# Performance work log

Measured on AMD Instinct MI355X. Metric: run time of the kernel, lower is better.

## Reference

```python
import jax, jax.numpy as jnp
import numpy as np
from jax.scipy.linalg import expm

DIM = 64
TIMESTEPS = 1000
BATCH = 1024


def setup_inputs() -> dict:
    key = jax.random.key(0)
    k1, k2 = jax.random.split(key)
    inputs = jax.random.normal(k1, (BATCH, TIMESTEPS, DIM), dtype=jnp.float32)
    # Kernel: skew-symmetric (oscillatory) + small decay so expm(kernel*t) stays
    # bounded for t up to TIMESTEPS-1 (a random dense kernel would overflow).
    a = jax.random.normal(k2, (DIM, DIM), dtype=jnp.float32)
    kernel = 0.01 * (a - a.T) - 0.002 * jnp.eye(DIM, dtype=jnp.float32)
    return {"inputs": inputs, "kernel": kernel}


def reference(inputs, kernel):
    # matrix_exponentials[t] = expm(kernel * t), t = 0..T-1  -> [T, dim, dim]
    ts = jnp.arange(TIMESTEPS, dtype=kernel.dtype)
    mexp = jax.vmap(expm)(kernel[None, :, :] * ts[:, None, None])
    # trajs = einsum('tij,bj->bti'): propagate initial state inputs[:, 0, :]
    x0 = inputs[:, 0, :]  # [B, dim]
    return jnp.einsum('tij,bj->bti', mexp, x0)  # [B, T, dim]
```

## Files before the change

### kernel.cpp

```cpp
#include <hip/hip_runtime.h>

#define NMAT 1000
#define SA_PAD 68
#define LDM 72

typedef short short8 __attribute__((ext_vector_type(8)));
typedef float floatx4 __attribute__((ext_vector_type(4)));
typedef unsigned short ushortx4 __attribute__((ext_vector_type(4)));

__device__ __forceinline__ unsigned short f2bf(float f) {
    unsigned int u = __float_as_uint(f);
    u += 0x7fffu + ((u >> 16) & 1u);
    return (unsigned short)(u >> 16);
}

__device__ __forceinline__ void mm_core(const float* __restrict__ sA,
                                        const float* __restrict__ sB,
                                        int r0, int c0, float acc[4][4])
{
#pragma unroll
    for (int k = 0; k < 64; k += 4) {
        float4 b0 = *(const float4*)&sB[(k + 0) * SA_PAD + c0];
        float4 b1 = *(const float4*)&sB[(k + 1) * SA_PAD + c0];
        float4 b2 = *(const float4*)&sB[(k + 2) * SA_PAD + c0];
        float4 b3 = *(const float4*)&sB[(k + 3) * SA_PAD + c0];
#pragma unroll
        for (int u = 0; u < 4; ++u) {
            float4 a = *(const float4*)&sA[(r0 + u) * SA_PAD + k];
            acc[u][0] += a.x * b0.x + a.y * b1.x + a.z * b2.x + a.w * b3.x;
            acc[u][1] += a.x * b0.y + a.y * b1.y + a.z * b2.y + a.w * b3.y;
            acc[u][2] += a.x * b0.z + a.y * b1.z + a.z * b2.z + a.w * b3.z;
            acc[u][3] += a.x * b0.w + a.y * b1.w + a.z * b2.w + a.w * b3.w;
        }
    }
}

__device__ __forceinline__ void stageLDS(float* __restrict__ s, const float* __restrict__ g, int tid)
{
#pragma unroll
    for (int q = 0; q < 4; ++q) {
        int i4 = tid + 256 * q;
        int r = i4 >> 4, c4 = (i4 & 15) * 4;
        *(float4*)&s[r * SA_PAD + c4] = *(const float4*)&g[i4 * 4];
    }
}

__global__ __launch_bounds__(256) void k_build(const float* __restrict__ K,
                                               float* __restrict__ ws)
{
    __shared__ __align__(16) float smem[6 * 64 * SA_PAD];
    float* tab = ws;
    const int tid = threadIdx.x;

#pragma unroll
    for (int q = 0; q < 4; ++q) {
        int i4 = tid + 256 * q;
        int r = i4 >> 4, c4 = (i4 & 15) * 4;
        *(float4*)&smem[r * SA_PAD + c4] = *(const float4*)&K[i4 * 4];
        float4 id = {0.f, 0.f, 0.f, 0.f};
        if (r >= c4 && r < c4 + 4) ((float*)&id)[r - c4] = 1.f;
        *(float4*)&tab[r * 64 + c4] = id;
    }

    const float c1_ = 1.f, c2_ = 0.5f, c3_ = 1.f / 6.f, c4_ = 1.f / 24.f, c5_ = 1.f / 120.f,
                c6_ = 1.f / 720.f, c7_ = 1.f / 5040.f, c8_ = 1.f / 40320.f, c9_ = 1.f / 362880.f,
                c10_ = 1.f / 3628800.f, c11_ = 1.f / 39916800.f, c12_ = 1.f / 479001600.f;

    const signed char SD[14]  = {1, 2, 3, 5, 4, 5, 0, 1, 2, 3, 4, 5, 0, 1};
    const signed char SAi[14] = {0, 1, 1, 4, 5, 4, 5, 0, 1, 2, 3, 4, 5, 0};
    const signed char SBi[14] = {0, 0, 1, 3, 3, 4, 5, 0, 1, 2, 3, 4, 5, 0};
    const signed char SE[14]  = {-1, -1, -1, 0, 1, -1, -1, -1, -1, -1, -1, -1, -1, -1};
    const short       STt[14] = {-1, -1, -1, -1, 1, 2, 4, 8, 16, 32, 64, 128, 256, 512};

    const int r0 = (tid >> 4) * 4, c0 = (tid & 15) * 4;

#pragma unroll 1
    for (int st = 0; st < 14; ++st) {
        if (st == 3) {
            __syncthreads();
#pragma unroll
            for (int s = 0; s < 16; ++s) {
                int idx = tid + 256 * s;
                int r = idx >> 6, c = idx & 63;
                smem[4 * (64 * SA_PAD) + r * SA_PAD + c] =
                      c12_ * smem[3 * (64 * SA_PAD) + r * SA_PAD + c] + (r == c ? c8_ : 0.f)
                    + c9_  * smem[0 * (64 * SA_PAD) + r * SA_PAD + c]
                    + c10_ * smem[1 * (64 * SA_PAD) + r * SA_PAD + c]
                    + c11_ * smem[2 * (64 * SA_PAD) + r * SA_PAD + c];
            }
        }
        __syncthreads();
        const float* A = smem + (int)SAi[st] * (64 * SA_PAD);
        const float* B = smem + (int)SBi[st] * (64 * SA_PAD);
        float acc[4][4] = {};
        mm_core(A, B, r0, c0, acc);

        float cI = 0.f, cK = 0.f, cT2 = 0.f, cT3 = 0.f;
        const int epi = SE[st];
        if (epi == 0) { cI = c4_; cK = c5_; cT2 = c6_; cT3 = c7_; }
        if (epi == 1) { cI = 1.f; cK = c1_; cT2 = c2_; cT3 = c3_; }

        float* D = smem + (int)SD[st] * (64 * SA_PAD);
        float* tp = (STt[st] >= 0) ? (tab + (size_t)STt[st] * 4096) : nullptr;
#pragma unroll
        for (int u = 0; u < 4; ++u) {
            int r = r0 + u;
            float o[4];
#pragma unroll
            for (int v = 0; v < 4; ++v) {
                int c = c0 + v;
                float val = acc[u][v];
                if (epi >= 0) {
                    val += (r == c ? cI : 0.f)
                         + cK  * smem[0 * (64 * SA_PAD) + r * SA_PAD + c]
                         + cT2 * smem[1 * (64 * SA_PAD) + r * SA_PAD + c]
                         + cT3 * smem[2 * (64 * SA_PAD) + r * SA_PAD + c];
                }
                o[v] = val;
            }
            float4 vv = {o[0], o[1], o[2], o[3]};
            *(float4*)&D[r * SA_PAD + c0] = vv;
            if (tp) *(float4*)&tp[r * 64 + c0] = vv;
        }
    }
}

__global__ __launch_bounds__(256) void k_pows(float* __restrict__ ws)
{
    __shared__ __align__(16) float s0[64 * SA_PAD], s1[64 * SA_PAD], s2[64 * SA_PAD];
    const int t = blockIdx.x;
    if (__popc(t) < 2) return;
    float* tab = ws;
    const int tid = threadIdx.x;
    const int r0 = (tid >> 4) * 4, c0 = (tid & 15) * 4;

    float* P = s0;
    float* Bs = s1;
    float* Cs = s2;

    int hb = 31 - __clz(t);
    stageLDS(P, tab + (size_t)(1 << hb) * 4096, tid);
    int rem = t & ~(1 << hb);

    while (rem) {
        int b = 31 - __clz(rem);
        rem &= ~(1 << b);
        stageLDS(Bs, tab + (size_t)(1 << b) * 4096, tid);
        __syncthreads();
        float acc[4][4] = {};
        mm_core(P, Bs, r0, c0, acc);
        if (rem) {
#pragma unroll
            for (int u = 0; u < 4; ++u) {
                float4 vv = {acc[u][0], acc[u][1], acc[u][2], acc[u][3]};
                *(float4*)&Cs[(r0 + u) * SA_PAD + c0] = vv;
            }
        } else {
            float* C = tab + (size_t)t * 4096;
#pragma unroll
            for (int u = 0; u < 4; ++u) {
                float4 vv = {acc[u][0], acc[u][1], acc[u][2], acc[u][3]};
                *(float4*)&C[(r0 + u) * 64 + c0] = vv;
            }
        }
        __syncthreads();
        if (rem) { float* tmp = P; P = Cs; Cs = tmp; }
    }
}

__global__ __launch_bounds__(256) void k_out(const float* __restrict__ in,
                                             const float* __restrict__ ws,
                                             float* __restrict__ out)
{
    __shared__ __align__(16) unsigned short lM[64 * LDM];
    __shared__ __align__(16) unsigned short lX[128 * LDM];

    const int bx = blockIdx.x;
    const int t = bx >> 3;
    const int b0 = (bx & 7) * 128;
    const float* Mt = ws + (size_t)t * 4096;
    const int tid = threadIdx.x;

#pragma unroll
    for (int q = 0; q < 4; ++q) {
        int i4 = tid + 256 * q;
        int i = i4 >> 4, c4 = (i4 & 15) * 4;
        float4 v = *(const float4*)&Mt[i4 * 4];
        ushortx4 h = { f2bf(v.x), f2bf(v.y), f2bf(v.z), f2bf(v.w) };
        *(ushortx4*)&lM[i * LDM + c4] = h;
    }
#pragma unroll
    for (int q = 0; q < 8; ++q) {
        int i4 = tid + 256 * q;
        int bb = i4 >> 4, c4 = (i4 & 15) * 4;
        float4 v = *(const float4*)&in[(size_t)(b0 + bb) * 64000 + c4];
        ushortx4 h = { f2bf(v.x), f2bf(v.y), f2bf(v.z), f2bf(v.w) };
        *(ushortx4*)&lX[bb * LDM + c4] = h;
    }
    __syncthreads();

    const int lane = tid & 63;
    const int w = tid >> 6;
    const int m = lane & 15;
    const int kg = lane >> 4;

#pragma unroll
    for (int mt = 0; mt < 2; ++mt) {
        const int mtile = w * 2 + mt;
        short8 a0 = *(const short8*)&lX[(mtile * 16 + m) * LDM + kg * 8];
        short8 a1 = *(const short8*)&lX[(mtile * 16 + m) * LDM + 32 + kg * 8];
#pragma unroll
        for (int n = 0; n < 4; ++n) {
            short8 bf0 = *(const short8*)&lM[(n * 16 + m) * LDM + kg * 8];
            short8 bf1 = *(const short8*)&lM[(n * 16 + m) * LDM + 32 + kg * 8];
            floatx4 acc = {0.f, 0.f, 0.f, 0.f};
            acc = __builtin_amdgcn_mfma_f32_16x16x32_bf16(a0, bf0, acc, 0, 0, 0);
            acc = __builtin_amdgcn_mfma_f32_16x16x32_bf16(a1, bf1, acc, 0, 0, 0);
            size_t base = (size_t)(b0 + mtile * 16 + kg * 4) * 64000 + (size_t)t * 64 + n * 16 + m;
            out[base + 0 * 64000] = acc[0];
            out[base + 1 * 64000] = acc[1];
            out[base + 2 * 64000] = acc[2];
            out[base + 3 * 64000] = acc[3];
        }
    }
}

extern "C" void kernel_launch(void* const* d_in, const int* in_sizes, int n_in,
                              void* d_out, int out_size, void* d_ws, size_t ws_size,
                              hipStream_t stream)
{
    const float* inp = (const float*)d_in[0];
    const float* K   = (const float*)d_in[1];
    float* out = (float*)d_out;
    float* ws  = (float*)d_ws;

    hipLaunchKernelGGL(k_build, dim3(1), dim3(256), 0, stream, K, ws);
    hipLaunchKernelGGL(k_pows, dim3(NMAT), dim3(256), 0, stream, ws);
    hipLaunchKernelGGL(k_out, dim3(8000), dim3(256), 0, stream, inp, ws, out);
}
```

Before: 614.0 us.

## Store matrix table and x0 as bf16 in workspace, prefetch seeds in pows

The power table is now stored in bf16, and a separate fp32 seed buffer holds the power-of-two matrices used by k_pows. Extra blocks in k_build convert the x0 rows to bf16 once, so k_out's 8000 blocks read compact bf16 data without reconverting. k_pows also register-prefetches the next seed factor while the current multiply runs. The aim is to cut global traffic and redundant conversion in k_out, at the cost of more workspace layout complexity.

```diff
diff --git a/kernel.cpp b/kernel.cpp
--- a/kernel.cpp
+++ b/kernel.cpp
@@ -3,6 +3,9 @@
 #define NMAT 1000
 #define SA_PAD 68
 #define LDM 72
+
+#define SEEDF_OFF 2048000
+#define X0B_OFF   8355840
 
 typedef short short8 __attribute__((ext_vector_type(8)));
 typedef float floatx4 __attribute__((ext_vector_type(4)));
@@ -46,20 +49,36 @@
 }
 
 __global__ __launch_bounds__(256) void k_build(const float* __restrict__ K,
+                                               const float* __restrict__ in,
                                                float* __restrict__ ws)
 {
+    const int tid = threadIdx.x;
+    unsigned short* tab16 = (unsigned short*)ws;
+    unsigned short* x0b = (unsigned short*)((char*)ws + X0B_OFF);
+
+    if (blockIdx.x != 0) {
+        const int rb = (blockIdx.x - 1) * 64;
+#pragma unroll
+        for (int q = 0; q < 4; ++q) {
+            int i4 = tid + 256 * q;
+            int b = rb + (i4 >> 4), c4 = (i4 & 15) * 4;
+            float4 v = *(const float4*)&in[(size_t)b * 64000 + c4];
+            ushortx4 h = { f2bf(v.x), f2bf(v.y), f2bf(v.z), f2bf(v.w) };
+            *(ushortx4*)&x0b[(size_t)b * 64 + c4] = h;
+        }
+        return;
+    }
+
     __shared__ __align__(16) float smem[6 * 64 * SA_PAD];
-    float* tab = ws;
-    const int tid = threadIdx.x;
 
 #pragma unroll
     for (int q = 0; q < 4; ++q) {
         int i4 = tid + 256 * q;
         int r = i4 >> 4, c4 = (i4 & 15) * 4;
         *(float4*)&smem[r * SA_PAD + c4] = *(const float4*)&K[i4 * 4];
-        float4 id = {0.f, 0.f, 0.f, 0.f};
-        if (r >= c4 && r < c4 + 4) ((float*)&id)[r - c4] = 1.f;
-        *(float4*)&tab[r * 64 + c4] = id;
+        ushortx4 id = {0, 0, 0, 0};
+        if (r >= c4 && r < c4 + 4) ((unsigned short*)&id)[r - c4] = 0x3F80;
+        *(ushortx4*)&tab16[r * 64 + c4] = id;
     }
 
     const float c1_ = 1.f, c2_ = 0.5f, c3_ = 1.f / 6.f, c4_ = 1.f / 24.f, c5_ = 1.f / 120.f,
@@ -101,7 +120,8 @@
         if (epi == 1) { cI = 1.f; cK = c1_; cT2 = c2_; cT3 = c3_; }
 
         float* D = smem + (int)SD[st] * (64 * SA_PAD);
-        float* tp = (STt[st] >= 0) ? (tab + (size_t)STt[st] * 4096) : nullptr;
+        float* sf = (STt[st] >= 0) ? (ws + SEEDF_OFF + (size_t)(st - 4) * 4096) : nullptr;
+        unsigned short* tb = (STt[st] >= 0) ? (tab16 + (size_t)STt[st] * 4096) : nullptr;
 #pragma unroll
         for (int u = 0; u < 4; ++u) {
             int r = r0 + u;
@@ -120,7 +140,11 @@
             }
             float4 vv = {o[0], o[1], o[2], o[3]};
             *(float4*)&D[r * SA_PAD + c0] = vv;
-            if (tp) *(float4*)&tp[r * 64 + c0] = vv;
+            if (sf) {
+                *(float4*)&sf[r * 64 + c0] = vv;
+                ushortx4 h = { f2bf(o[0]), f2bf(o[1]), f2bf(o[2]), f2bf(o[3]) };
+                *(ushortx4*)&tb[r * 64 + c0] = h;
+            }
         }
     }
 }
@@ -130,7 +154,8 @@
     __shared__ __align__(16) float s0[64 * SA_PAD], s1[64 * SA_PAD], s2[64 * SA_PAD];
     const int t = blockIdx.x;
     if (__popc(t) < 2) return;
-    float* tab = ws;
+    const float* seedF = ws + SEEDF_OFF;
+    unsigned short* tab16 = (unsigned short*)ws;
     const int tid = threadIdx.x;
     const int r0 = (tid >> 4) * 4, c0 = (tid & 15) * 4;
 
@@ -139,63 +164,83 @@
     float* Cs = s2;
 
     int hb = 31 - __clz(t);
-    stageLDS(P, tab + (size_t)(1 << hb) * 4096, tid);
+    stageLDS(P, seedF + (size_t)hb * 4096, tid);
     int rem = t & ~(1 << hb);
 
-    while (rem) {
+    float4 rg[4];
+    {
         int b = 31 - __clz(rem);
         rem &= ~(1 << b);
-        stageLDS(Bs, tab + (size_t)(1 << b) * 4096, tid);
+        const float* g = seedF + (size_t)b * 4096;
+#pragma unroll
+        for (int q = 0; q < 4; ++q) rg[q] = *(const float4*)&g[(tid + 256 * q) * 4];
+    }
+
+    while (true) {
+        __syncthreads();
+#pragma unroll
+        for (int q = 0; q < 4; ++q) {
+            int i4 = tid + 256 * q;
+            int rr = i4 >> 4, c4 = (i4 & 15) * 4;
+            *(float4*)&Bs[rr * SA_PAD + c4] = rg[q];
+        }
+        int nb = -1;
+        if (rem) {
+            nb = 31 - __clz(rem);
+            rem &= ~(1 << nb);
+            const float* g = seedF + (size_t)nb * 4096;
+#pragma unroll
+            for (int q = 0; q < 4; ++q) rg[q] = *(const float4*)&g[(tid + 256 * q) * 4];
+        }
         __syncthreads();
         float acc[4][4] = {};
         mm_core(P, Bs, r0, c0, acc);
-        if (rem) {
+
+        if (nb < 0) {
+            unsigned short* C = tab16 + (size_t)t * 4096;
 #pragma unroll
             for (int u = 0; u < 4; ++u) {
-                float4 vv = {acc[u][0], acc[u][1], acc[u][2], acc[u][3]};
-                *(float4*)&Cs[(r0 + u) * SA_PAD + c0] = vv;
-            }
-        } else {
-            float* C = tab + (size_t)t * 4096;
-#pragma unroll
-            for (int u = 0; u < 4; ++u) {
-                float4 vv = {acc[u][0], acc[u][1], acc[u][2], acc[u][3]};
-                *(float4*)&C[(r0 + u) * 64 + c0] = vv;
-            }
-        }
-        __syncthreads();
-        if (rem) { float* tmp = P; P = Cs; Cs = tmp; }
-    }
-}
-
-__global__ __launch_bounds__(256) void k_out(const float* __restrict__ in,
-                                             const float* __restrict__ ws,
+                ushortx4 h = { f2bf(acc[u][0]), f2bf(acc[u][1]),
+                               f2bf(acc[u][2]), f2bf(acc[u][3]) };
+                *(ushortx4*)&C[(r0 + u) * 64 + c0] = h;
+            }
+            return;
+        }
+#pragma unroll
+        for (int u = 0; u < 4; ++u) {
+            float4 vv = {acc[u][0], acc[u][1], acc[u][2], acc[u][3]};
+            *(float4*)&Cs[(r0 + u) * SA_PAD + c0] = vv;
+        }
+        float* tmp = P; P = Cs; Cs = tmp;
+    }
+}
+
+__global__ __launch_bounds__(256) void k_out(const float* __restrict__ ws,
                                              float* __restrict__ out)
 {
     __shared__ __align__(16) unsigned short lM[64 * LDM];
     __shared__ __align__(16) unsigned short lX[128 * LDM];
+
+    const unsigned short* tab16 = (const unsigned short*)ws;
+    const unsigned short* x0b = (const unsigned short*)((const char*)ws + X0B_OFF);
 
     const int bx = blockIdx.x;
     const int t = bx >> 3;
     const int b0 = (bx & 7) * 128;
-    const float* Mt = ws + (size_t)t * 4096;
+    const unsigned short* Mt = tab16 + (size_t)t * 4096;
     const int tid = threadIdx.x;
 
 #pragma unroll
+    for (int q = 0; q < 2; ++q) {
+        int i8 = tid + 256 * q;
+        int i = i8 >> 3, j8 = (i8 & 7) * 8;
+        *(short8*)&lM[i * LDM + j8] = *(const short8*)&Mt[i8 * 8];
+    }
+#pragma unroll
     for (int q = 0; q < 4; ++q) {
-        int i4 = tid + 256 * q;
-        int i = i4 >> 4, c4 = (i4 & 15) * 4;
-        float4 v = *(const float4*)&Mt[i4 * 4];
-        ushortx4 h = { f2bf(v.x), f2bf(v.y), f2bf(v.z), f2bf(v.w) };
-        *(ushortx4*)&lM[i * LDM + c4] = h;
-    }
-#pragma unroll
-    for (int q = 0; q < 8; ++q) {
-        int i4 = tid + 256 * q;
-        int bb = i4 >> 4, c4 = (i4 & 15) * 4;
-        float4 v = *(const float4*)&in[(size_t)(b0 + bb) * 64000 + c4];
-        ushortx4 h = { f2bf(v.x), f2bf(v.y), f2bf(v.z), f2bf(v.w) };
-        *(ushortx4*)&lX[bb * LDM + c4] = h;
+        int i8 = tid + 256 * q;
+        int bb = i8 >> 3, j8 = (i8 & 7) * 8;
+        *(short8*)&lX[bb * LDM + j8] = *(const short8*)&x0b[(size_t)(b0 + bb) * 64 + j8];
     }
     __syncthreads();
 
@@ -234,7 +279,7 @@
     float* out = (float*)d_out;
     float* ws  = (float*)d_ws;
 
-    hipLaunchKernelGGL(k_build, dim3(1), dim3(256), 0, stream, K, ws);
+    hipLaunchKernelGGL(k_build, dim3(17), dim3(256), 0, stream, K, inp, ws);
     hipLaunchKernelGGL(k_pows, dim3(NMAT), dim3(256), 0, stream, ws);
-    hipLaunchKernelGGL(k_out, dim3(8000), dim3(256), 0, stream, inp, ws, out);
-}
+    hipLaunchKernelGGL(k_out, dim3(8000), dim3(256), 0, stream, ws, out);
+}
```

After: 590.8 us. 1.04x faster.
